# Kernel tuning notes

Measured on AMD Instinct MI355X. Metric: run time of the kernel, lower is better.

## Reference

```python
import jax, jax.numpy as jnp
import numpy as np

N_NODES = 50000
N_EDGES = 600000
N_GRAPHS = 512
LN_EPS = 1e-5


def setup_inputs() -> dict:
    key = jax.random.key(0)
    ks = jax.random.split(key, 18)
    s = 0.05
    return {
        "x": jax.random.normal(ks[0], (N_NODES, 29), jnp.float32),
        "xdims": jax.random.normal(ks[1], (N_NODES, 3), jnp.float32),
        "xsttype": jax.random.randint(ks[2], (N_NODES,), 0, 256),
        "edge_index": jax.random.randint(ks[3], (2, N_EDGES), 0, N_NODES),
        "batch": jnp.sort(jax.random.randint(ks[4], (N_NODES,), 0, N_GRAPHS)),
        "st_emb": jax.random.normal(ks[5], (256, 12), jnp.float32) * s,
        "Wl1": jax.random.normal(ks[6], (128, 44), jnp.float32) * s,
        "bl1": jnp.zeros((128,), jnp.float32),
        "Wr1": jax.random.normal(ks[7], (128, 44), jnp.float32) * s,
        "g1": jnp.ones((128,), jnp.float32),
        "beta1": jnp.zeros((128,), jnp.float32),
        "Wl2": jax.random.normal(ks[8], (128, 128), jnp.float32) * s,
        "bl2": jnp.zeros((128,), jnp.float32),
        "Wr2": jax.random.normal(ks[9], (128, 128), jnp.float32) * s,
        "g2": jnp.ones((128,), jnp.float32),
        "beta2": jnp.zeros((128,), jnp.float32),
        "Wlin": jax.random.normal(ks[10], (10, 256), jnp.float32) * s,
        "blin": jnp.zeros((10,), jnp.float32),
    }


def layernorm(h, g, b):
    mu = jnp.mean(h, axis=-1, keepdims=True)
    var = jnp.mean(jnp.square(h - mu), axis=-1, keepdims=True)
    return g * (h - mu) * jax.lax.rsqrt(var + LN_EPS) + b


def sage_conv(h, src, dst, Wl, bl, Wr):
    # PyG SAGEConv: lin_l(mean_j x_j) + lin_r(x_i); messages flow src -> dst.
    msg = h[src]                                            # [E, D]
    agg = jax.ops.segment_sum(msg, dst, num_segments=N_NODES)
    cnt = jax.ops.segment_sum(jnp.ones((msg.shape[0],), h.dtype), dst, num_segments=N_NODES)
    mean = agg / jnp.maximum(cnt, 1.0)[:, None]
    return mean @ Wl.T + bl + h @ Wr.T


def reference(x, xdims, xsttype, edge_index, batch, st_emb,
              Wl1, bl1, Wr1, g1, beta1,
              Wl2, bl2, Wr2, g2, beta2,
              Wlin, blin):
    src, dst = edge_index[0], edge_index[1]
    h = jnp.concatenate([x, xdims, st_emb[xsttype]], axis=1)   # [N, 44]
    # Layer 1
    h = jax.nn.relu(layernorm(sage_conv(h, src, dst, Wl1, bl1, Wr1), g1, beta1))
    # Layer 2
    h = jax.nn.relu(layernorm(sage_conv(h, src, dst, Wl2, bl2, Wr2), g2, beta2))
    # dropout inactive (inference)
    hs = jax.ops.segment_sum(h, batch, num_segments=N_GRAPHS)
    nc = jax.ops.segment_sum(jnp.ones((h.shape[0],), h.dtype), batch, num_segments=N_GRAPHS)
    hmean = hs / jnp.maximum(nc, 1.0)[:, None]
    hmax = jax.ops.segment_max(h, batch, num_segments=N_GRAPHS)
    pooled = jnp.concatenate([hmean, hmax], axis=1)            # [G, 256]
    return pooled @ Wlin.T + blin                              # [G, 10]
```

## Files before the change

### kernel.cpp

```cpp
#include <hip/hip_runtime.h>
#include <hip/hip_bf16.h>
#include <math.h>

#define N_NODES 50000
#define N_EDGES 600000
#define N_GRAPHS 512
#define LN_EPS 1e-5f
#define CAP 64
#define CSTRIDE 16
#define EDGE_BLOCKS ((N_EDGES / 4 + 255) / 256)
#define PREP_BLOCKS ((N_NODES * 8 + 255) / 256)

typedef short bf16x8 __attribute__((ext_vector_type(8)));
typedef float f32x4 __attribute__((ext_vector_type(4)));

__device__ __forceinline__ unsigned short f2bf(float f) {
    unsigned int x = __float_as_uint(f);
    return (unsigned short)((x + 0x7fffu + ((x >> 16) & 1u)) >> 16);
}
__device__ __forceinline__ float bflo(unsigned int u) { return __uint_as_float(u << 16); }
__device__ __forceinline__ float bfhi(unsigned int u) { return __uint_as_float(u & 0xffff0000u); }

__global__ __launch_bounds__(256) void zero_kernel(int* __restrict__ cntp)
{
    int i = blockIdx.x * 256 + threadIdx.x;
    if (i < N_NODES * CSTRIDE) cntp[i] = 0;
}

__global__ __launch_bounds__(256) void prep_fill_kernel(
    const float* __restrict__ x, const float* __restrict__ xdims,
    const int* __restrict__ stt, const float* __restrict__ st_emb,
    const float* __restrict__ Wl1, const float* __restrict__ Wr1,
    const float* __restrict__ Wl2, const float* __restrict__ Wr2,
    const int* __restrict__ batch,
    const int* __restrict__ esrc_in, const int* __restrict__ edst_in,
    unsigned short* __restrict__ Xh1, unsigned short* __restrict__ Wc1,
    unsigned short* __restrict__ Wc2, int* __restrict__ cntp,
    unsigned short* __restrict__ adj, int* __restrict__ starts)
{
    if (blockIdx.x < EDGE_BLOCKS) {
        int t = blockIdx.x * 256 + threadIdx.x;
        int e4 = t * 4;
        if (e4 < N_EDGES) {
            int4 d4 = *(const int4*)(edst_in + e4);
            int4 s4 = *(const int4*)(esrc_in + e4);
            int sl0 = atomicAdd(&cntp[d4.x * CSTRIDE], 1);
            int sl1 = atomicAdd(&cntp[d4.y * CSTRIDE], 1);
            int sl2 = atomicAdd(&cntp[d4.z * CSTRIDE], 1);
            int sl3 = atomicAdd(&cntp[d4.w * CSTRIDE], 1);
            if (sl0 < CAP) adj[(size_t)d4.x * CAP + sl0] = (unsigned short)s4.x;
            if (sl1 < CAP) adj[(size_t)d4.y * CAP + sl1] = (unsigned short)s4.y;
            if (sl2 < CAP) adj[(size_t)d4.z * CAP + sl2] = (unsigned short)s4.z;
            if (sl3 < CAP) adj[(size_t)d4.w * CAP + sl3] = (unsigned short)s4.w;
        }
        return;
    }
    int idx = (blockIdx.x - EDGE_BLOCKS) * 256 + threadIdx.x;

    if (idx < N_NODES * 8) {
        int n = idx >> 3;
        int c0 = (idx & 7) * 8;
        float vv[8];
        #pragma unroll
        for (int j = 0; j < 8; ++j) {
            int c = c0 + j;
            float v;
            if (c < 29)       v = x[n * 29 + c];
            else if (c < 32)  v = xdims[n * 3 + (c - 29)];
            else if (c < 44)  v = st_emb[stt[n] * 12 + (c - 32)];
            else              v = 0.f;
            vv[j] = v;
        }
        uint4 p;
        p.x = (unsigned int)f2bf(vv[0]) | ((unsigned int)f2bf(vv[1]) << 16);
        p.y = (unsigned int)f2bf(vv[2]) | ((unsigned int)f2bf(vv[3]) << 16);
        p.z = (unsigned int)f2bf(vv[4]) | ((unsigned int)f2bf(vv[5]) << 16);
        p.w = (unsigned int)f2bf(vv[6]) | ((unsigned int)f2bf(vv[7]) << 16);
        ((uint4*)Xh1)[idx] = p;
    }
    if (idx < 128 * 128) {
        int f = idx >> 7, k = idx & 127;
        float v;
        if (k < 44)        v = Wr1[f * 44 + k];
        else if (k < 64)   v = 0.f;
        else if (k < 108)  v = Wl1[f * 44 + (k - 64)];
        else               v = 0.f;
        Wc1[idx] = f2bf(v);
    }
    if (idx < 128 * 256) {
        int f = idx >> 8, k = idx & 255;
        float v = (k < 128) ? Wr2[f * 128 + k] : Wl2[f * 128 + (k - 128)];
        Wc2[idx] = f2bf(v);
    }
    if (idx < N_NODES) {
        int b = batch[idx];
        int pb = (idx == 0) ? -1 : batch[idx - 1];
        for (int g = pb + 1; g <= b; ++g) starts[g] = idx;
        if (idx == N_NODES - 1)
            for (int g = b + 1; g <= N_GRAPHS; ++g) starts[g] = N_NODES;
    }
}

template <int DHALF>
__global__ __launch_bounds__(256) void agg_kernel(const int* __restrict__ cntp,
                                                  const unsigned short* __restrict__ adj,
                                                  const unsigned short* __restrict__ Xh,
                                                  unsigned short* __restrict__ M)
{
    constexpr int CH = DHALF / 8;
    constexpr int NG = 64 / CH;
    constexpr int NL = 16 / NG;
    int n = blockIdx.x * 4 + (threadIdx.x >> 6);
    if (n >= N_NODES) return;
    const int lane = threadIdx.x & 63;
    const int grp = lane / CH;
    const int sl  = lane % CH;
    int degT = cntp[n * CSTRIDE];
    int deg  = (degT < CAP) ? degT : CAP;
    int er = (int)adj[(size_t)n * CAP + lane];
    float a0=0.f,a1=0.f,a2=0.f,a3=0.f,a4=0.f,a5=0.f,a6=0.f,a7=0.f;
    const uint4* gbase = (const uint4*)Xh;
    const int c1 = deg - 1;
    for (int e = 0; e < deg; e += 16) {
        uint4 v[NL]; float mk[NL];
        #pragma unroll
        for (int j = 0; j < NL; ++j) {
            int ee = e + j * NG + grp;
            int s = __shfl(er, (ee < c1) ? ee : c1);
            v[j]  = gbase[(size_t)s * CH + sl];
            mk[j] = (ee < deg) ? 1.f : 0.f;
        }
        #pragma unroll
        for (int j = 0; j < NL; ++j) {
            a0 += mk[j] * bflo(v[j].x); a1 += mk[j] * bfhi(v[j].x);
            a2 += mk[j] * bflo(v[j].y); a3 += mk[j] * bfhi(v[j].y);
            a4 += mk[j] * bflo(v[j].z); a5 += mk[j] * bfhi(v[j].z);
            a6 += mk[j] * bflo(v[j].w); a7 += mk[j] * bfhi(v[j].w);
        }
    }
    #pragma unroll
    for (int m = CH; m <= 32; m <<= 1) {
        a0 += __shfl_xor(a0, m); a1 += __shfl_xor(a1, m);
        a2 += __shfl_xor(a2, m); a3 += __shfl_xor(a3, m);
        a4 += __shfl_xor(a4, m); a5 += __shfl_xor(a5, m);
        a6 += __shfl_xor(a6, m); a7 += __shfl_xor(a7, m);
    }
    if (grp == 0) {
        float inv = (degT > 0) ? 1.f / (float)degT : 0.f;
        uint4 p;
        p.x = (unsigned int)f2bf(a0 * inv) | ((unsigned int)f2bf(a1 * inv) << 16);
        p.y = (unsigned int)f2bf(a2 * inv) | ((unsigned int)f2bf(a3 * inv) << 16);
        p.z = (unsigned int)f2bf(a4 * inv) | ((unsigned int)f2bf(a5 * inv) << 16);
        p.w = (unsigned int)f2bf(a6 * inv) | ((unsigned int)f2bf(a7 * inv) << 16);
        ((uint4*)M)[(size_t)n * CH + sl] = p;
    }
}

template <int KPAD>
__global__ __launch_bounds__(256) void mfma_layer_kernel(
    const unsigned short* __restrict__ Xh, const unsigned short* __restrict__ M,
    const unsigned short* __restrict__ W,
    const float* __restrict__ bl, const float* __restrict__ g,
    const float* __restrict__ beta,
    unsigned short* __restrict__ Out)
{
    constexpr int DHALF = KPAD / 2;
    const int lane = threadIdx.x & 63;
    const int wv   = threadIdx.x >> 6;
    const int l15  = lane & 15;
    const int l4   = lane >> 4;
    const int row0 = blockIdx.x * 128 + wv * 32;

    int rA0 = row0 + l15;       if (rA0 > N_NODES - 1) rA0 = N_NODES - 1;
    int rA1 = row0 + 16 + l15;  if (rA1 > N_NODES - 1) rA1 = N_NODES - 1;

    f32x4 acc[2][8];
    #pragma unroll
    for (int m = 0; m < 2; ++m)
        #pragma unroll
        for (int n = 0; n < 8; ++n) acc[m][n] = (f32x4){0.f, 0.f, 0.f, 0.f};

    const int kb = l4 * 8;
    #pragma unroll
    for (int ks = 0; ks < KPAD / 32; ++ks) {
        const int k = ks * 32 + kb;
        bf16x8 a0, a1;
        if (ks < DHALF / 32) {
            a0 = *(const bf16x8*)(Xh + (size_t)rA0 * DHALF + k);
            a1 = *(const bf16x8*)(Xh + (size_t)rA1 * DHALF + k);
        } else {
            a0 = *(const bf16x8*)(M + (size_t)rA0 * DHALF + (k - DHALF));
            a1 = *(const bf16x8*)(M + (size_t)rA1 * DHALF + (k - DHALF));
        }
        #pragma unroll
        for (int ni = 0; ni < 8; ++ni) {
            bf16x8 b = *(const bf16x8*)(W + (size_t)(ni * 16 + l15) * KPAD + k);
            acc[0][ni] = __builtin_amdgcn_mfma_f32_16x16x32_bf16(a0, b, acc[0][ni], 0, 0, 0);
            acc[1][ni] = __builtin_amdgcn_mfma_f32_16x16x32_bf16(a1, b, acc[1][ni], 0, 0, 0);
        }
    }

    float blv[8], gv[8], bev[8];
    #pragma unroll
    for (int ni = 0; ni < 8; ++ni) {
        int f = ni * 16 + l15;
        blv[ni] = bl[f]; gv[ni] = g[f]; bev[ni] = beta[f];
    }

    #pragma unroll
    for (int mi = 0; mi < 2; ++mi) {
        #pragma unroll
        for (int r = 0; r < 4; ++r) {
            float v[8];
            float s1 = 0.f, s2 = 0.f;
            #pragma unroll
            for (int ni = 0; ni < 8; ++ni) {
                float t = acc[mi][ni][r] + blv[ni];
                v[ni] = t; s1 += t; s2 += t * t;
            }
            #pragma unroll
            for (int m = 8; m >= 1; m >>= 1) {
                s1 += __shfl_xor(s1, m);
                s2 += __shfl_xor(s2, m);
            }
            float mu   = s1 * (1.f / 128.f);
            float var  = s2 * (1.f / 128.f) - mu * mu;
            float rstd = rsqrtf(var + LN_EPS);
            int node = row0 + mi * 16 + l4 * 4 + r;
            if (node < N_NODES) {
                #pragma unroll
                for (int ni = 0; ni < 8; ++ni) {
                    float o = gv[ni] * (v[ni] - mu) * rstd + bev[ni];
                    o = fmaxf(o, 0.f);
                    Out[(size_t)node * 128 + ni * 16 + l15] = f2bf(o);
                }
            }
        }
    }
}

__global__ __launch_bounds__(256) void poolhead_kernel(const unsigned short* __restrict__ h2,
                                                       const int* __restrict__ starts,
                                                       const float* __restrict__ Wlin,
                                                       const float* __restrict__ blin,
                                                       float* __restrict__ out)
{
    const int g  = blockIdx.x;
    const int j2 = threadIdx.x & 63;
    const int h  = threadIdx.x >> 6;
    const int s0 = starts[g], s1 = starts[g + 1];
    float sa = 0.f, sb = 0.f, ma = -INFINITY, mb = -INFINITY;
    const unsigned int* base = (const unsigned int*)h2;
    int n = s0 + h;
    for (; n + 4 < s1; n += 8) {
        unsigned int u0 = base[(size_t)n * 64 + j2];
        unsigned int u1 = base[(size_t)(n + 4) * 64 + j2];
        float l0 = bflo(u0), h0 = bfhi(u0);
        float l1 = bflo(u1), h1 = bfhi(u1);
        sa += l0 + l1; sb += h0 + h1;
        ma = fmaxf(ma, fmaxf(l0, l1));
        mb = fmaxf(mb, fmaxf(h0, h1));
    }
    if (n < s1) {
        unsigned int u = base[(size_t)n * 64 + j2];
        float lo = bflo(u), hi = bfhi(u);
        sa += lo; sb += hi;
        ma = fmaxf(ma, lo); mb = fmaxf(mb, hi);
    }
    __shared__ float red[4][4][64];
    __shared__ float pooled[256];
    red[h][0][j2] = sa; red[h][1][j2] = sb; red[h][2][j2] = ma; red[h][3][j2] = mb;
    __syncthreads();
    if (h == 0) {
        #pragma unroll
        for (int o = 1; o < 4; ++o) {
            sa += red[o][0][j2]; sb += red[o][1][j2];
            ma = fmaxf(ma, red[o][2][j2]); mb = fmaxf(mb, red[o][3][j2]);
        }
        int c = s1 - s0;
        float inv = (c > 0) ? 1.f / (float)c : 0.f;
        pooled[2 * j2]           = sa * inv;
        pooled[2 * j2 + 1]       = sb * inv;
        pooled[128 + 2 * j2]     = (c > 0) ? ma : 0.f;
        pooled[128 + 2 * j2 + 1] = (c > 0) ? mb : 0.f;
    }
    __syncthreads();
    if (threadIdx.x < 10) {
        const float* w = Wlin + threadIdx.x * 256;
        float acc = blin[threadIdx.x];
        for (int k = 0; k < 256; ++k) acc += pooled[k] * w[k];
        out[g * 10 + threadIdx.x] = acc;
    }
}

extern "C" void kernel_launch(void* const* d_in, const int* in_sizes, int n_in,
                              void* d_out, int out_size, void* d_ws, size_t ws_size,
                              hipStream_t stream)
{
    const float* x      = (const float*)d_in[0];
    const float* xdims  = (const float*)d_in[1];
    const int*   stt    = (const int*)d_in[2];
    const int*   eidx   = (const int*)d_in[3];
    const int*   batch  = (const int*)d_in[4];
    const float* st_emb = (const float*)d_in[5];
    const float* Wl1 = (const float*)d_in[6];
    const float* bl1 = (const float*)d_in[7];
    const float* Wr1 = (const float*)d_in[8];
    const float* g1  = (const float*)d_in[9];
    const float* be1 = (const float*)d_in[10];
    const float* Wl2 = (const float*)d_in[11];
    const float* bl2 = (const float*)d_in[12];
    const float* Wr2 = (const float*)d_in[13];
    const float* g2  = (const float*)d_in[14];
    const float* be2 = (const float*)d_in[15];
    const float* Wlin = (const float*)d_in[16];
    const float* blin = (const float*)d_in[17];
    float* out = (float*)d_out;

    const int* esrc_in = eidx;
    const int* edst_in = eidx + N_EDGES;

    char* ws = (char*)d_ws;
    size_t o = 0;
    auto carve = [&](size_t bytes) { void* p = ws + o; o = (o + bytes + 255) & ~(size_t)255; return p; };
    unsigned short* Xh1  = (unsigned short*)carve((size_t)N_NODES * 64 * 2);
    unsigned short* M1   = (unsigned short*)carve((size_t)N_NODES * 64 * 2);
    unsigned short* Xh2  = (unsigned short*)carve((size_t)N_NODES * 128 * 2);
    unsigned short* M2   = (unsigned short*)carve((size_t)N_NODES * 128 * 2);
    unsigned short* h2bf = (unsigned short*)carve((size_t)N_NODES * 128 * 2);
    unsigned short* Wc1  = (unsigned short*)carve((size_t)128 * 128 * 2);
    unsigned short* Wc2  = (unsigned short*)carve((size_t)128 * 256 * 2);
    int*            cntp = (int*)carve((size_t)N_NODES * CSTRIDE * 4);
    unsigned short* adj  = (unsigned short*)carve((size_t)N_NODES * CAP * 2);
    int*          starts = (int*)carve((size_t)(N_GRAPHS + 1) * 4);
    (void)ws_size;

    zero_kernel<<<(N_NODES * CSTRIDE + 255) / 256, 256, 0, stream>>>(cntp);

    prep_fill_kernel<<<EDGE_BLOCKS + PREP_BLOCKS, 256, 0, stream>>>(
        x, xdims, stt, st_emb, Wl1, Wr1, Wl2, Wr2, batch,
        esrc_in, edst_in, Xh1, Wc1, Wc2, cntp, adj, starts);

    agg_kernel<64><<<(N_NODES + 3) / 4, 256, 0, stream>>>(cntp, adj, Xh1, M1);
    mfma_layer_kernel<128><<<(N_NODES + 127) / 128, 256, 0, stream>>>(
        Xh1, M1, Wc1, bl1, g1, be1, Xh2);

    agg_kernel<128><<<(N_NODES + 3) / 4, 256, 0, stream>>>(cntp, adj, Xh2, M2);
    mfma_layer_kernel<256><<<(N_NODES + 127) / 128, 256, 0, stream>>>(
        Xh2, M2, Wc2, bl2, g2, be2, h2bf);

    poolhead_kernel<<<N_GRAPHS, 256, 0, stream>>>(h2bf, starts, Wlin, blin, out);
}
```

Baseline: 131.9 us.

## Build adjacency via two-pass destination binning with shared-memory atomics

Replaces the per-edge global atomic fill of the padded adjacency list with a two-pass scheme. Edges are first bucketed into 128-node bins using block-local shared atomics, with one global atomic per bin per block. A per-bin kernel then builds the adjacency rows with shared-memory atomics. This removes the large zero kernel and the padded count array, and cuts contended global atomics and scattered writes, at the cost of an extra kernel launch, an intermediate bin buffer, and a fixed per-bin capacity that can drop edges if a bin overflows.

```diff
diff --git a/kernel.cpp b/kernel.cpp
--- a/kernel.cpp
+++ b/kernel.cpp
@@ -7,8 +7,10 @@
 #define N_GRAPHS 512
 #define LN_EPS 1e-5f
 #define CAP 64
-#define CSTRIDE 16
-#define EDGE_BLOCKS ((N_EDGES / 4 + 255) / 256)
+#define NPB 128
+#define NBINS ((N_NODES + NPB - 1) / NPB)
+#define BCAP 2048
+#define BPAD 16
 #define PREP_BLOCKS ((N_NODES * 8 + 255) / 256)
 
 typedef short bf16x8 __attribute__((ext_vector_type(8)));
@@ -21,41 +23,17 @@
 __device__ __forceinline__ float bflo(unsigned int u) { return __uint_as_float(u << 16); }
 __device__ __forceinline__ float bfhi(unsigned int u) { return __uint_as_float(u & 0xffff0000u); }
 
-__global__ __launch_bounds__(256) void zero_kernel(int* __restrict__ cntp)
-{
-    int i = blockIdx.x * 256 + threadIdx.x;
-    if (i < N_NODES * CSTRIDE) cntp[i] = 0;
-}
-
-__global__ __launch_bounds__(256) void prep_fill_kernel(
+__global__ __launch_bounds__(256) void prep_kernel(
     const float* __restrict__ x, const float* __restrict__ xdims,
     const int* __restrict__ stt, const float* __restrict__ st_emb,
     const float* __restrict__ Wl1, const float* __restrict__ Wr1,
     const float* __restrict__ Wl2, const float* __restrict__ Wr2,
     const int* __restrict__ batch,
-    const int* __restrict__ esrc_in, const int* __restrict__ edst_in,
     unsigned short* __restrict__ Xh1, unsigned short* __restrict__ Wc1,
-    unsigned short* __restrict__ Wc2, int* __restrict__ cntp,
-    unsigned short* __restrict__ adj, int* __restrict__ starts)
-{
-    if (blockIdx.x < EDGE_BLOCKS) {
-        int t = blockIdx.x * 256 + threadIdx.x;
-        int e4 = t * 4;
-        if (e4 < N_EDGES) {
-            int4 d4 = *(const int4*)(edst_in + e4);
-            int4 s4 = *(const int4*)(esrc_in + e4);
-            int sl0 = atomicAdd(&cntp[d4.x * CSTRIDE], 1);
-            int sl1 = atomicAdd(&cntp[d4.y * CSTRIDE], 1);
-            int sl2 = atomicAdd(&cntp[d4.z * CSTRIDE], 1);
-            int sl3 = atomicAdd(&cntp[d4.w * CSTRIDE], 1);
-            if (sl0 < CAP) adj[(size_t)d4.x * CAP + sl0] = (unsigned short)s4.x;
-            if (sl1 < CAP) adj[(size_t)d4.y * CAP + sl1] = (unsigned short)s4.y;
-            if (sl2 < CAP) adj[(size_t)d4.z * CAP + sl2] = (unsigned short)s4.z;
-            if (sl3 < CAP) adj[(size_t)d4.w * CAP + sl3] = (unsigned short)s4.w;
-        }
-        return;
-    }
-    int idx = (blockIdx.x - EDGE_BLOCKS) * 256 + threadIdx.x;
+    unsigned short* __restrict__ Wc2, int* __restrict__ binCnt,
+    int* __restrict__ starts)
+{
+    int idx = blockIdx.x * 256 + threadIdx.x;
 
     if (idx < N_NODES * 8) {
         int n = idx >> 3;
@@ -99,10 +77,74 @@
         if (idx == N_NODES - 1)
             for (int g = b + 1; g <= N_GRAPHS; ++g) starts[g] = N_NODES;
     }
+    if (idx < NBINS * BPAD) binCnt[idx] = 0;
+}
+
+__global__ __launch_bounds__(1024) void bin_scatter_kernel(
+    const int* __restrict__ esrc_in, const int* __restrict__ edst_in,
+    int* __restrict__ binCnt, unsigned int* __restrict__ binBuf)
+{
+    __shared__ int cntL[NBINS];
+    __shared__ int gbaseL[NBINS];
+    const int tid = threadIdx.x;
+    for (int i = tid; i < NBINS; i += 1024) cntL[i] = 0;
+    __syncthreads();
+
+    int e4 = (blockIdx.x * 1024 + tid) * 4;
+    int4 d4, s4; int b0=0,b1=0,b2=0,b3=0, r0=0,r1=0,r2=0,r3=0;
+    const bool valid = e4 < N_EDGES;
+    if (valid) {
+        d4 = *(const int4*)(edst_in + e4);
+        s4 = *(const int4*)(esrc_in + e4);
+        b0 = d4.x >> 7; b1 = d4.y >> 7; b2 = d4.z >> 7; b3 = d4.w >> 7;
+        r0 = atomicAdd(&cntL[b0], 1);
+        r1 = atomicAdd(&cntL[b1], 1);
+        r2 = atomicAdd(&cntL[b2], 1);
+        r3 = atomicAdd(&cntL[b3], 1);
+    }
+    __syncthreads();
+    for (int i = tid; i < NBINS; i += 1024) {
+        int c = cntL[i];
+        gbaseL[i] = (c > 0) ? atomicAdd(&binCnt[i * BPAD], c) : 0;
+    }
+    __syncthreads();
+    if (valid) {
+        int p0 = gbaseL[b0] + r0, p1 = gbaseL[b1] + r1;
+        int p2 = gbaseL[b2] + r2, p3 = gbaseL[b3] + r3;
+        if (p0 < BCAP) binBuf[(size_t)b0 * BCAP + p0] = (((unsigned)d4.x & 127u) << 16) | (unsigned)s4.x;
+        if (p1 < BCAP) binBuf[(size_t)b1 * BCAP + p1] = (((unsigned)d4.y & 127u) << 16) | (unsigned)s4.y;
+        if (p2 < BCAP) binBuf[(size_t)b2 * BCAP + p2] = (((unsigned)d4.z & 127u) << 16) | (unsigned)s4.z;
+        if (p3 < BCAP) binBuf[(size_t)b3 * BCAP + p3] = (((unsigned)d4.w & 127u) << 16) | (unsigned)s4.w;
+    }
+}
+
+__global__ __launch_bounds__(256) void bin_adj_kernel(
+    const int* __restrict__ binCnt, const unsigned int* __restrict__ binBuf,
+    unsigned short* __restrict__ adj, int* __restrict__ cnt)
+{
+    __shared__ int cl[NPB];
+    const int b = blockIdx.x;
+    const int tid = threadIdx.x;
+    if (tid < NPB) cl[tid] = 0;
+    __syncthreads();
+    int ec = binCnt[b * BPAD]; if (ec > BCAP) ec = BCAP;
+    const unsigned int* buf = binBuf + (size_t)b * BCAP;
+    for (int i = tid; i < ec; i += 256) {
+        unsigned int p = buf[i];
+        int dl = (int)(p >> 16);
+        int slot = atomicAdd(&cl[dl], 1);
+        if (slot < CAP)
+            adj[((size_t)(b * NPB + dl)) * CAP + slot] = (unsigned short)(p & 0xFFFFu);
+    }
+    __syncthreads();
+    if (tid < NPB) {
+        int n = b * NPB + tid;
+        if (n < N_NODES) cnt[n] = cl[tid];
+    }
 }
 
 template <int DHALF>
-__global__ __launch_bounds__(256) void agg_kernel(const int* __restrict__ cntp,
+__global__ __launch_bounds__(256) void agg_kernel(const int* __restrict__ cnt,
                                                   const unsigned short* __restrict__ adj,
                                                   const unsigned short* __restrict__ Xh,
                                                   unsigned short* __restrict__ M)
@@ -115,7 +157,7 @@
     const int lane = threadIdx.x & 63;
     const int grp = lane / CH;
     const int sl  = lane % CH;
-    int degT = cntp[n * CSTRIDE];
+    int degT = cnt[n];
     int deg  = (degT < CAP) ? degT : CAP;
     int er = (int)adj[(size_t)n * CAP + lane];
     float a0=0.f,a1=0.f,a2=0.f,a3=0.f,a4=0.f,a5=0.f,a6=0.f,a7=0.f;
@@ -330,22 +372,27 @@
     unsigned short* h2bf = (unsigned short*)carve((size_t)N_NODES * 128 * 2);
     unsigned short* Wc1  = (unsigned short*)carve((size_t)128 * 128 * 2);
     unsigned short* Wc2  = (unsigned short*)carve((size_t)128 * 256 * 2);
-    int*            cntp = (int*)carve((size_t)N_NODES * CSTRIDE * 4);
-    unsigned short* adj  = (unsigned short*)carve((size_t)N_NODES * CAP * 2);
+    int*            cnt  = (int*)carve((size_t)N_NODES * 4);
+    int*          binCnt = (int*)carve((size_t)NBINS * BPAD * 4);
+    unsigned int* binBuf = (unsigned int*)carve((size_t)NBINS * BCAP * 4);
+    unsigned short* adj  = (unsigned short*)carve((size_t)(NBINS * NPB) * CAP * 2);
     int*          starts = (int*)carve((size_t)(N_GRAPHS + 1) * 4);
     (void)ws_size;
 
-    zero_kernel<<<(N_NODES * CSTRIDE + 255) / 256, 256, 0, stream>>>(cntp);
-
-    prep_fill_kernel<<<EDGE_BLOCKS + PREP_BLOCKS, 256, 0, stream>>>(
+    prep_kernel<<<PREP_BLOCKS, 256, 0, stream>>>(
         x, xdims, stt, st_emb, Wl1, Wr1, Wl2, Wr2, batch,
-        esrc_in, edst_in, Xh1, Wc1, Wc2, cntp, adj, starts);
-
-    agg_kernel<64><<<(N_NODES + 3) / 4, 256, 0, stream>>>(cntp, adj, Xh1, M1);
+        Xh1, Wc1, Wc2, binCnt, starts);
+
+    bin_scatter_kernel<<<(N_EDGES / 4 + 1023) / 1024, 1024, 0, stream>>>(
+        esrc_in, edst_in, binCnt, binBuf);
+
+    bin_adj_kernel<<<NBINS, 256, 0, stream>>>(binCnt, binBuf, adj, cnt);
+
+    agg_kernel<64><<<(N_NODES + 3) / 4, 256, 0, stream>>>(cnt, adj, Xh1, M1);
     mfma_layer_kernel<128><<<(N_NODES + 127) / 128, 256, 0, stream>>>(
         Xh1, M1, Wc1, bl1, g1, be1, Xh2);
 
-    agg_kernel<128><<<(N_NODES + 3) / 4, 256, 0, stream>>>(cntp, adj, Xh2, M2);
+    agg_kernel<128><<<(N_NODES + 3) / 4, 256, 0, stream>>>(cnt, adj, Xh2, M2);
     mfma_layer_kernel<256><<<(N_NODES + 127) / 128, 256, 0, stream>>>(
         Xh2, M2, Wc2, bl2, g2, be2, h2bf);
 
```

After: 116.1 us. -12.0%, faster.
